# Kernel optimization log

Measured on AMD Instinct MI355X. Metric: run time of the kernel, lower is better.

## Reference

```python
import jax, jax.numpy as jnp
import numpy as np
from math import sqrt

POOL = 8  # pool_size from init_kwargs


def setup_inputs() -> dict:
    key = jax.random.key(0)
    k1, k2, k3 = jax.random.split(key, 3)
    b, c, h, w = 16, 64, 256, 256
    dim_k = 64
    x = jax.random.normal(k1, (b, c, h, w), dtype=jnp.float32)
    # torch nn.Linear(num_feat, dim_k, bias=False) weight: (dim_k, num_feat)
    bound = 1.0 / sqrt(c)
    Wq = jax.random.uniform(k2, (dim_k, c), minval=-bound, maxval=bound, dtype=jnp.float32)
    Wk = jax.random.uniform(k3, (dim_k, c), minval=-bound, maxval=bound, dtype=jnp.float32)
    return {"x": x, "Wq": Wq, "Wk": Wk}


def reference(x, Wq, Wk):
    p = POOL
    b, c, h, w = x.shape
    wh, ww = h // p, w // p  # window size
    n = p * p                # number of windows / pooled tokens
    dim_k = Wq.shape[0]
    scale = 1.0 / sqrt(dim_k)

    # AdaptiveAvgPool2d(p) with divisible dims == mean over (wh, ww) blocks
    y = x.reshape(b, c, p, wh, p, ww).mean(axis=(3, 5))  # (b, c, p, p)
    y = y.reshape(b, c, n).transpose(0, 2, 1)            # (b, n, c)

    q = jnp.einsum('bnc,kc->bnk', y, Wq)  # (b, n, dim_k)
    k = jnp.einsum('bnc,kc->bnk', y, Wk)  # (b, n, dim_k)

    # window_partition of x.permute(0,2,3,1) with window [wh, ww]
    xp = x.transpose(0, 2, 3, 1)                               # (b, h, w, c)
    v = xp.reshape(b, p, wh, p, ww, c)
    v = v.transpose(0, 1, 3, 2, 4, 5).reshape(b, n, wh * ww * c)  # (b, n, wh*ww*c)

    dist = jax.nn.softmax(jnp.einsum('bnk,bmk->bnm', q, k) * scale, axis=-1)  # (b, n, n)
    att = jnp.einsum('bnm,bmd->bnd', dist, v)  # (b, n, wh*ww*c)

    # window_reverse -> (b, h, w, c), then permute to (b, c, h, w)
    out = att.reshape(b, p, p, wh, ww, c)
    out = out.transpose(0, 1, 3, 2, 4, 5).reshape(b, h, w, c)
    return out.transpose(0, 3, 1, 2)
```

## Files before the change

kernel.cpp:

```cpp
#include <hip/hip_runtime.h>
#include <math.h>


__global__ __launch_bounds__(256) void pool_kernel(const float* __restrict__ x,
                                                   float* __restrict__ yT)
{
    int bc = blockIdx.x;
    int b  = bc >> 6, c = bc & 63;
    const float4* plane = (const float4*)(x + (size_t)bc * 65536);
    int t    = threadIdx.x;
    int col4 = t & 63;
    int q    = t >> 6;
    __shared__ float red[256];

    for (int wr = 0; wr < 8; ++wr) {
        float acc = 0.f;
#pragma unroll
        for (int it = 0; it < 8; ++it) {
            int row = wr * 32 + it * 4 + q;
            float4 v = plane[row * 64 + col4];
            acc += v.x + v.y + v.z + v.w;
        }
        red[t] = acc;
        __syncthreads();
        if (t < 8) {
            float s = 0.f;
#pragma unroll
            for (int qq = 0; qq < 4; ++qq)
#pragma unroll
                for (int ss = 0; ss < 8; ++ss)
                    s += red[qq * 64 + t * 8 + ss];
            int n = wr * 8 + t;
            yT[b * 4096 + c * 64 + n] = s * (1.0f / 1024.0f);
        }
        __syncthreads();
    }
}

#define ST 68
__global__ __launch_bounds__(256) void attn_kernel(const float* __restrict__ yT,
                                                   const float* __restrict__ Wq,
                                                   const float* __restrict__ Wk,
                                                   float* __restrict__ distT)
{
    __shared__ float ylT[64 * ST];
    __shared__ float wqT[64 * ST];
    __shared__ float wkT[64 * ST];
    __shared__ float qlT[64 * ST];
    __shared__ float klT[64 * ST];
    __shared__ float sT [64 * ST];
    int b = blockIdx.x, t = threadIdx.x;

#pragma unroll
    for (int o = 0; o < 16; ++o) {
        int idx = o * 256 + t;
        int r = idx >> 6, cl = idx & 63;
        ylT[r * ST + cl] = yT[b * 4096 + idx];
        wqT[cl * ST + r] = Wq[idx];
        wkT[cl * ST + r] = Wk[idx];
    }
    __syncthreads();

    int lane = t & 63, ng = t >> 6;

    float qa[16], ka[16];
#pragma unroll
    for (int i = 0; i < 16; ++i) { qa[i] = 0.f; ka[i] = 0.f; }
    for (int c = 0; c < 64; ++c) {
        float wq = wqT[c * ST + lane];
        float wk = wkT[c * ST + lane];
        const float4* yr = (const float4*)(ylT + c * ST + ng * 16);
        float4 y0 = yr[0], y1 = yr[1], y2 = yr[2], y3 = yr[3];
        qa[0]  += y0.x * wq; qa[1]  += y0.y * wq; qa[2]  += y0.z * wq; qa[3]  += y0.w * wq;
        qa[4]  += y1.x * wq; qa[5]  += y1.y * wq; qa[6]  += y1.z * wq; qa[7]  += y1.w * wq;
        qa[8]  += y2.x * wq; qa[9]  += y2.y * wq; qa[10] += y2.z * wq; qa[11] += y2.w * wq;
        qa[12] += y3.x * wq; qa[13] += y3.y * wq; qa[14] += y3.z * wq; qa[15] += y3.w * wq;
        ka[0]  += y0.x * wk; ka[1]  += y0.y * wk; ka[2]  += y0.z * wk; ka[3]  += y0.w * wk;
        ka[4]  += y1.x * wk; ka[5]  += y1.y * wk; ka[6]  += y1.z * wk; ka[7]  += y1.w * wk;
        ka[8]  += y2.x * wk; ka[9]  += y2.y * wk; ka[10] += y2.z * wk; ka[11] += y2.w * wk;
        ka[12] += y3.x * wk; ka[13] += y3.y * wk; ka[14] += y3.z * wk; ka[15] += y3.w * wk;
    }
    {
        float4* qd = (float4*)(qlT + lane * ST + ng * 16);
        float4* kd = (float4*)(klT + lane * ST + ng * 16);
        qd[0] = make_float4(qa[0],  qa[1],  qa[2],  qa[3]);
        qd[1] = make_float4(qa[4],  qa[5],  qa[6],  qa[7]);
        qd[2] = make_float4(qa[8],  qa[9],  qa[10], qa[11]);
        qd[3] = make_float4(qa[12], qa[13], qa[14], qa[15]);
        kd[0] = make_float4(ka[0],  ka[1],  ka[2],  ka[3]);
        kd[1] = make_float4(ka[4],  ka[5],  ka[6],  ka[7]);
        kd[2] = make_float4(ka[8],  ka[9],  ka[10], ka[11]);
        kd[3] = make_float4(ka[12], ka[13], ka[14], ka[15]);
    }
    __syncthreads();

    float s[16];
#pragma unroll
    for (int i = 0; i < 16; ++i) s[i] = 0.f;
    for (int d = 0; d < 64; ++d) {
        float kv = klT[d * ST + lane];
        const float4* qr = (const float4*)(qlT + d * ST + ng * 16);
        float4 q0 = qr[0], q1 = qr[1], q2 = qr[2], q3 = qr[3];
        s[0]  += q0.x * kv; s[1]  += q0.y * kv; s[2]  += q0.z * kv; s[3]  += q0.w * kv;
        s[4]  += q1.x * kv; s[5]  += q1.y * kv; s[6]  += q1.z * kv; s[7]  += q1.w * kv;
        s[8]  += q2.x * kv; s[9]  += q2.y * kv; s[10] += q2.z * kv; s[11] += q2.w * kv;
        s[12] += q3.x * kv; s[13] += q3.y * kv; s[14] += q3.z * kv; s[15] += q3.w * kv;
    }
    const float scale = 0.125f;
#pragma unroll
    for (int i = 0; i < 16; ++i) {
        float v = s[i] * scale;
        float mx = v;
        mx = fmaxf(mx, __shfl_xor(mx, 1));
        mx = fmaxf(mx, __shfl_xor(mx, 2));
        mx = fmaxf(mx, __shfl_xor(mx, 4));
        mx = fmaxf(mx, __shfl_xor(mx, 8));
        mx = fmaxf(mx, __shfl_xor(mx, 16));
        mx = fmaxf(mx, __shfl_xor(mx, 32));
        float e = expf(v - mx);
        float sm = e;
        sm += __shfl_xor(sm, 1);
        sm += __shfl_xor(sm, 2);
        sm += __shfl_xor(sm, 4);
        sm += __shfl_xor(sm, 8);
        sm += __shfl_xor(sm, 16);
        sm += __shfl_xor(sm, 32);
        s[i] = e / sm;
    }
    {
        float4* sd = (float4*)(sT + lane * ST + ng * 16);
        sd[0] = make_float4(s[0],  s[1],  s[2],  s[3]);
        sd[1] = make_float4(s[4],  s[5],  s[6],  s[7]);
        sd[2] = make_float4(s[8],  s[9],  s[10], s[11]);
        sd[3] = make_float4(s[12], s[13], s[14], s[15]);
    }
    __syncthreads();

#pragma unroll
    for (int o = 0; o < 16; ++o) {
        int idx = o * 256 + t;
        int m = idx >> 6, n = idx & 63;
        distT[b * 4096 + idx] = sT[m * ST + n];
    }
}

#define XL_ISTRIDE 2052
__global__ __launch_bounds__(256) void combine_kernel(const float* __restrict__ x,
                                                      const float* __restrict__ distT,
                                                      float* __restrict__ out)
{
    __shared__ float Dt[4096];
    __shared__ float Xl[4 * XL_ISTRIDE];
    int blk = blockIdx.x;
    int ig  = blk & 7;
    int bc  = blk >> 3;
    int b   = bc >> 6;
    const float* plane  = x   + (size_t)bc * 65536;
    float*       oplane = out + (size_t)bc * 65536;
    const float* dT     = distT + b * 4096;
    int t = threadIdx.x;

    for (int o = 0; o < 16; ++o) Dt[o * 256 + t] = dT[o * 256 + t];

    float4* Xl4 = (float4*)Xl;
    const float4* plane4 = (const float4*)plane;
#pragma unroll
    for (int o = 0; o < 8; ++o) {
        int f4        = o * 256 + t;
        int row_local = f4 >> 6;
        int col4      = f4 & 63;
        int i         = row_local >> 3;
        int m_row     = row_local & 7;
        int g_row     = m_row * 32 + ig * 4 + i;
        Xl4[i * (XL_ISTRIDE / 4) + m_row * 64 + col4] = plane4[g_row * 64 + col4];
    }
    __syncthreads();

    int j4 = t & 7;
    int i  = (t >> 3) & 3;
    int tg = t >> 5;
    const float4* Xr = (const float4*)Xl + i * (XL_ISTRIDE / 4) + j4;
    const float4* Dr = (const float4*)Dt + tg * 2;

    float4 acc[8];
#pragma unroll
    for (int r = 0; r < 8; ++r) acc[r] = make_float4(0.f, 0.f, 0.f, 0.f);

#pragma unroll 8
    for (int m = 0; m < 64; ++m) {
        int m_row = m >> 3, m_col = m & 7;
        float4 v  = Xr[m_row * 64 + m_col * 8];
        float4 d0 = Dr[m * 16];
        float4 d1 = Dr[m * 16 + 1];
        acc[0].x += d0.x * v.x; acc[0].y += d0.x * v.y; acc[0].z += d0.x * v.z; acc[0].w += d0.x * v.w;
        acc[1].x += d0.y * v.x; acc[1].y += d0.y * v.y; acc[1].z += d0.y * v.z; acc[1].w += d0.y * v.w;
        acc[2].x += d0.z * v.x; acc[2].y += d0.z * v.y; acc[2].z += d0.z * v.z; acc[2].w += d0.z * v.w;
        acc[3].x += d0.w * v.x; acc[3].y += d0.w * v.y; acc[3].z += d0.w * v.z; acc[3].w += d0.w * v.w;
        acc[4].x += d1.x * v.x; acc[4].y += d1.x * v.y; acc[4].z += d1.x * v.z; acc[4].w += d1.x * v.w;
        acc[5].x += d1.y * v.x; acc[5].y += d1.y * v.y; acc[5].z += d1.y * v.z; acc[5].w += d1.y * v.w;
        acc[6].x += d1.z * v.x; acc[6].y += d1.z * v.y; acc[6].z += d1.z * v.z; acc[6].w += d1.z * v.w;
        acc[7].x += d1.w * v.x; acc[7].y += d1.w * v.y; acc[7].z += d1.w * v.z; acc[7].w += d1.w * v.w;
    }

    float4* orow = (float4*)(oplane + (tg * 32 + ig * 4 + i) * 256) + j4;
#pragma unroll
    for (int r = 0; r < 8; ++r) orow[r * 8] = acc[r];
}

extern "C" void kernel_launch(void* const* d_in, const int* in_sizes, int n_in,
                              void* d_out, int out_size, void* d_ws, size_t ws_size,
                              hipStream_t stream)
{
    const float* x  = (const float*)d_in[0];
    const float* Wq = (const float*)d_in[1];
    const float* Wk = (const float*)d_in[2];
    float* out = (float*)d_out;

    float* y_ws  = (float*)d_ws;
    float* distT = y_ws + 65536;

    pool_kernel   <<<1024, 256, 0, stream>>>(x, y_ws);
    attn_kernel   <<<16,   256, 0, stream>>>(y_ws, Wq, Wk, distT);
    combine_kernel<<<8192, 256, 0, stream>>>(x, distT, out);
}
```

Measured before the change: 532.9 us.

## Reverse combine block order, use nontemporal stores, and batch pool reductions

The pool kernel now issues all eight window-row loads first and does a single shared-memory reduction with one barrier, instead of syncing eight times. The combine kernel walks planes in reverse order so the planes the pool kernel read last, likely still in cache, are consumed first. It also loads the attention matrix with float4 and writes the output with nontemporal stores so the output does not evict cached input. The risks are higher register pressure in the pool kernel and nontemporal-store behavior that depends on the hardware.

```diff
diff --git a/kernel.cpp b/kernel.cpp
--- a/kernel.cpp
+++ b/kernel.cpp
@@ -1,6 +1,8 @@
 #include <hip/hip_runtime.h>
 #include <math.h>
 
+
+typedef float nfloat4 __attribute__((ext_vector_type(4)));
 
 __global__ __launch_bounds__(256) void pool_kernel(const float* __restrict__ x,
                                                    float* __restrict__ yT)
@@ -11,29 +13,35 @@
     int t    = threadIdx.x;
     int col4 = t & 63;
     int q    = t >> 6;
-    __shared__ float red[256];
-
+
+    float acc[8];
+#pragma unroll
+    for (int wr = 0; wr < 8; ++wr) acc[wr] = 0.f;
+
+#pragma unroll
     for (int wr = 0; wr < 8; ++wr) {
-        float acc = 0.f;
 #pragma unroll
         for (int it = 0; it < 8; ++it) {
             int row = wr * 32 + it * 4 + q;
             float4 v = plane[row * 64 + col4];
-            acc += v.x + v.y + v.z + v.w;
+            acc[wr] += v.x + v.y + v.z + v.w;
         }
-        red[t] = acc;
-        __syncthreads();
-        if (t < 8) {
-            float s = 0.f;
-#pragma unroll
-            for (int qq = 0; qq < 4; ++qq)
-#pragma unroll
-                for (int ss = 0; ss < 8; ++ss)
-                    s += red[qq * 64 + t * 8 + ss];
-            int n = wr * 8 + t;
-            yT[b * 4096 + c * 64 + n] = s * (1.0f / 1024.0f);
-        }
-        __syncthreads();
+    }
+
+    __shared__ float red[8][264];
+#pragma unroll
+    for (int wr = 0; wr < 8; ++wr) red[wr][t] = acc[wr];
+    __syncthreads();
+
+    if (t < 64) {
+        int wr = t >> 3, wc = t & 7;
+        float s = 0.f;
+#pragma unroll
+        for (int qq = 0; qq < 4; ++qq)
+#pragma unroll
+            for (int ss = 0; ss < 8; ++ss)
+                s += red[wr][qq * 64 + wc * 8 + ss];
+        yT[b * 4096 + c * 64 + t] = s * (1.0f / 1024.0f);
     }
 }
 
@@ -153,14 +161,19 @@
     __shared__ float Xl[4 * XL_ISTRIDE];
     int blk = blockIdx.x;
     int ig  = blk & 7;
-    int bc  = blk >> 3;
+    int bc  = 1023 - (blk >> 3);
     int b   = bc >> 6;
     const float* plane  = x   + (size_t)bc * 65536;
     float*       oplane = out + (size_t)bc * 65536;
     const float* dT     = distT + b * 4096;
     int t = threadIdx.x;
 
-    for (int o = 0; o < 16; ++o) Dt[o * 256 + t] = dT[o * 256 + t];
+    {
+        float4* Dt4 = (float4*)Dt;
+        const float4* dT4 = (const float4*)dT;
+#pragma unroll
+        for (int o = 0; o < 4; ++o) Dt4[o * 256 + t] = dT4[o * 256 + t];
+    }
 
     float4* Xl4 = (float4*)Xl;
     const float4* plane4 = (const float4*)plane;
@@ -202,9 +215,13 @@
         acc[7].x += d1.w * v.x; acc[7].y += d1.w * v.y; acc[7].z += d1.w * v.z; acc[7].w += d1.w * v.w;
     }
 
-    float4* orow = (float4*)(oplane + (tg * 32 + ig * 4 + i) * 256) + j4;
-#pragma unroll
-    for (int r = 0; r < 8; ++r) orow[r * 8] = acc[r];
+    nfloat4* orow = (nfloat4*)((float*)(oplane + (tg * 32 + ig * 4 + i) * 256)) + j4;
+#pragma unroll
+    for (int r = 0; r < 8; ++r) {
+        nfloat4 v;
+        v.x = acc[r].x; v.y = acc[r].y; v.z = acc[r].z; v.w = acc[r].w;
+        __builtin_nontemporal_store(v, &orow[r * 8]);
+    }
 }
 
 extern "C" void kernel_launch(void* const* d_in, const int* in_sizes, int n_in,
```

Result: no change. 526.2 us (-1.3%).
